# Performance work log

Measured on AMD Instinct MI355X. Metric: run time of the kernel, lower is better.

The kernel has to match this reference:

```python
import jax, jax.numpy as jnp
import numpy as np

B = 1_000_000
D = 6
IU = jnp.triu_indices(D)  # upper-triangular index pair for 21-vector packing


def _make_pd_trivec(key, batch):
    # random PD covariance -> packed upper-triangular 21-vector
    A = 0.3 * jax.random.normal(key, (batch, D, D), dtype=jnp.float32)
    S = jnp.einsum('bij,bkj->bik', A, A) + jnp.eye(D, dtype=jnp.float32)
    return S[:, IU[0], IU[1]]  # [B, 21]


def _vec_to_sym(v):
    # [B,21] -> symmetric [B,6,6]
    M = jnp.zeros((v.shape[0], D, D), dtype=v.dtype).at[:, IU[0], IU[1]].set(v)
    diag = jnp.einsum('bii->bi', M)
    return M + jnp.swapaxes(M, -1, -2) - jnp.einsum('bi,ij->bij', diag, jnp.eye(D, dtype=v.dtype))


def setup_inputs() -> dict:
    key = jax.random.key(0)
    kt, kp = jax.random.split(key)
    return {
        'target': _make_pd_trivec(kt, B),
        'pred': _make_pd_trivec(kp, B),
    }


def reference(target, pred):
    # Huber loss (delta=1, mean reduction) on the packed vectors
    d = pred - target
    ad = jnp.abs(d)
    l1 = jnp.mean(jnp.where(ad < 1.0, 0.5 * d * d, ad - 0.5))

    eps_eye = 1e-5 * jnp.eye(D, dtype=pred.dtype)
    P = _vec_to_sym(pred) + eps_eye    # [B,6,6]
    T = _vec_to_sym(target) + eps_eye  # [B,6,6]

    # KL(N(0,P) || N(0,T)) = 0.5*(tr(T^-1 P) - 6 + logdet T - logdet P)
    Lp = jnp.linalg.cholesky(P)
    Lt = jnp.linalg.cholesky(T)
    solve = jax.vmap(lambda a, b: jax.scipy.linalg.solve_triangular(a, b, lower=True))
    M = solve(Lt, Lp)                               # Lt^{-1} Lp, [B,6,6]
    tr = jnp.sum(M * M, axis=(-1, -2))              # tr(T^-1 P)
    logdet_t = 2.0 * jnp.sum(jnp.log(jnp.einsum('bii->bi', Lt)), axis=-1)
    logdet_p = 2.0 * jnp.sum(jnp.log(jnp.einsum('bii->bi', Lp)), axis=-1)
    kl = 0.5 * (tr - D + logdet_t - logdet_p)

    return jnp.mean(kl) + l1
```

## Files before the change

kernel.cpp:

```cpp
#include <hip/hip_runtime.h>
#include <hip/hip_bf16.h>

#define B_TOTAL 1000000
#define NBLK2 ((B_TOTAL + 511) / 512)

typedef float f4u __attribute__((ext_vector_type(4), aligned(4)));

__device__ __forceinline__ constexpr int up_idx(int i, int j) {
    return i * 6 - i * (i - 1) / 2 + (j - i);
}

__device__ __forceinline__ void load21(const float* __restrict__ src, float* dst) {
#pragma unroll
    for (int q = 0; q < 5; ++q) {
        f4u v = *reinterpret_cast<const f4u*>(src + 4 * q);
        dst[4 * q + 0] = v[0]; dst[4 * q + 1] = v[1];
        dst[4 * q + 2] = v[2]; dst[4 * q + 3] = v[3];
    }
    dst[20] = src[20];
}

__device__ __forceinline__ void chol6(const float* v, float L[6][6], float dinv[6]) {
#pragma unroll
    for (int j = 0; j < 6; ++j) {
        float s = v[up_idx(j, j)] + 1e-5f;
#pragma unroll
        for (int k = 0; k < 6; ++k)
            if (k < j) s -= L[j][k] * L[j][k];
        float r = __builtin_amdgcn_rsqf(s);
        L[j][j] = s * r;
        dinv[j] = r;
#pragma unroll
        for (int i = 0; i < 6; ++i)
            if (i > j) {
                float a = v[up_idx(j, i)];
#pragma unroll
                for (int k = 0; k < 6; ++k)
                    if (k < j) a -= L[i][k] * L[j][k];
                L[i][j] = a * r;
            }
    }
}

__device__ __forceinline__ float element_loss(const float* t, const float* p) {
    float hs = 0.0f;
#pragma unroll
    for (int k = 0; k < 21; ++k) {
        float d = p[k] - t[k];
        float ad = fabsf(d);
        hs += (ad < 1.0f) ? 0.5f * d * d : ad - 0.5f;
    }

    float Lt[6][6], Lp[6][6], dti[6], dpi[6];
    chol6(t, Lt, dti);
    chol6(p, Lp, dpi);

    float tr = 0.0f;
#pragma unroll
    for (int c = 0; c < 6; ++c) {
        float m[6];
#pragma unroll
        for (int r = 0; r < 6; ++r)
            if (r >= c) {
                float s = Lp[r][c];
#pragma unroll
                for (int k = 0; k < 6; ++k)
                    if (k >= c && k < r) s -= Lt[r][k] * m[k];
                m[r] = s * dti[r];
                tr += m[r] * m[r];
            }
    }

    float ratio = 1.0f;
#pragma unroll
    for (int i = 0; i < 6; ++i) ratio *= Lt[i][i] * dpi[i];
    float kl = 0.5f * (tr - 6.0f) + 0.69314718056f * __builtin_amdgcn_logf(ratio);

    return kl + hs * (1.0f / 21.0f);
}

__global__ void __launch_bounds__(256) kl_huber_kernel(const float* __restrict__ target,
                                                       const float* __restrict__ pred,
                                                       double* __restrict__ partial) {
    const int tid = threadIdx.x;
    const long base = (long)blockIdx.x * 512;
    const long b0 = base + tid;
    const long b1 = base + 256 + tid;
    const bool valid0 = b0 < B_TOTAL;
    const bool valid1 = b1 < B_TOTAL;

    float t0[21], p0[21], t1[21], p1[21];
    if (valid0) {
        load21(target + b0 * 21, t0);
        load21(pred + b0 * 21, p0);
    }
    if (valid1) {
        load21(target + b1 * 21, t1);
        load21(pred + b1 * 21, p1);
    }

    float contrib = 0.0f;
    if (valid0) contrib += element_loss(t0, p0);
    if (valid1) contrib += element_loss(t1, p1);

#pragma unroll
    for (int off = 32; off > 0; off >>= 1) contrib += __shfl_down(contrib, off);

    __shared__ float wsum[4];
    int lane = tid & 63;
    int wid = tid >> 6;
    if (lane == 0) wsum[wid] = contrib;
    __syncthreads();
    if (tid == 0) {
        partial[blockIdx.x] = (double)(wsum[0] + wsum[1] + wsum[2] + wsum[3]);
    }
}

__global__ void __launch_bounds__(256) reduce_kernel(const double* __restrict__ partial,
                                                     float* __restrict__ out) {
    double s = 0.0;
    for (int i = threadIdx.x; i < NBLK2; i += 256) s += partial[i];
#pragma unroll
    for (int off = 32; off > 0; off >>= 1) s += __shfl_down(s, off);

    __shared__ double wsum[4];
    int lane = threadIdx.x & 63;
    int wid = threadIdx.x >> 6;
    if (lane == 0) wsum[wid] = s;
    __syncthreads();
    if (threadIdx.x == 0) {
        double total = wsum[0] + wsum[1] + wsum[2] + wsum[3];
        out[0] = (float)(total / (double)B_TOTAL);
    }
}

extern "C" void kernel_launch(void* const* d_in, const int* in_sizes, int n_in,
                              void* d_out, int out_size, void* d_ws, size_t ws_size,
                              hipStream_t stream) {
    const float* target = (const float*)d_in[0];
    const float* pred = (const float*)d_in[1];
    double* partial = (double*)d_ws;

    kl_huber_kernel<<<NBLK2, 256, 0, stream>>>(target, pred, partial);
    reduce_kernel<<<1, 256, 0, stream>>>(partial, (float*)d_out);
}
```

Measured before the change: 34.63 us.

## Process one element per thread with single-wavefront blocks

Each thread now handles one batch element instead of two, and blocks shrink to a single 64-lane wavefront, so the shared-memory cross-wave reduction and barrier go away. This lowers per-thread register demand and is meant to raise occupancy and latency hiding on loads. In exchange there are eight times more partial sums, so the single-block final reduction does more serial work.

```diff
diff --git a/kernel.cpp b/kernel.cpp
--- a/kernel.cpp
+++ b/kernel.cpp
@@ -2,7 +2,7 @@
 #include <hip/hip_bf16.h>
 
 #define B_TOTAL 1000000
-#define NBLK2 ((B_TOTAL + 511) / 512)
+#define NBLK64 ((B_TOTAL + 63) / 64)
 
 typedef float f4u __attribute__((ext_vector_type(4), aligned(4)));
 
@@ -79,47 +79,29 @@
     return kl + hs * (1.0f / 21.0f);
 }
 
-__global__ void __launch_bounds__(256) kl_huber_kernel(const float* __restrict__ target,
-                                                       const float* __restrict__ pred,
-                                                       double* __restrict__ partial) {
+__global__ void __launch_bounds__(64) kl_huber_kernel(const float* __restrict__ target,
+                                                      const float* __restrict__ pred,
+                                                      double* __restrict__ partial) {
     const int tid = threadIdx.x;
-    const long base = (long)blockIdx.x * 512;
-    const long b0 = base + tid;
-    const long b1 = base + 256 + tid;
-    const bool valid0 = b0 < B_TOTAL;
-    const bool valid1 = b1 < B_TOTAL;
-
-    float t0[21], p0[21], t1[21], p1[21];
-    if (valid0) {
-        load21(target + b0 * 21, t0);
-        load21(pred + b0 * 21, p0);
+    const long b = (long)blockIdx.x * 64 + tid;
+    float contrib = 0.0f;
+    if (b < B_TOTAL) {
+        float t[21], p[21];
+        load21(target + b * 21, t);
+        load21(pred + b * 21, p);
+        contrib = element_loss(t, p);
     }
-    if (valid1) {
-        load21(target + b1 * 21, t1);
-        load21(pred + b1 * 21, p1);
-    }
-
-    float contrib = 0.0f;
-    if (valid0) contrib += element_loss(t0, p0);
-    if (valid1) contrib += element_loss(t1, p1);
 
 #pragma unroll
     for (int off = 32; off > 0; off >>= 1) contrib += __shfl_down(contrib, off);
 
-    __shared__ float wsum[4];
-    int lane = tid & 63;
-    int wid = tid >> 6;
-    if (lane == 0) wsum[wid] = contrib;
-    __syncthreads();
-    if (tid == 0) {
-        partial[blockIdx.x] = (double)(wsum[0] + wsum[1] + wsum[2] + wsum[3]);
-    }
+    if (tid == 0) partial[blockIdx.x] = (double)contrib;
 }
 
 __global__ void __launch_bounds__(256) reduce_kernel(const double* __restrict__ partial,
                                                      float* __restrict__ out) {
     double s = 0.0;
-    for (int i = threadIdx.x; i < NBLK2; i += 256) s += partial[i];
+    for (int i = threadIdx.x; i < NBLK64; i += 256) s += partial[i];
 #pragma unroll
     for (int off = 32; off > 0; off >>= 1) s += __shfl_down(s, off);
 
@@ -141,6 +123,6 @@
     const float* pred = (const float*)d_in[1];
     double* partial = (double*)d_ws;
 
-    kl_huber_kernel<<<NBLK2, 256, 0, stream>>>(target, pred, partial);
+    kl_huber_kernel<<<NBLK64, 64, 0, stream>>>(target, pred, partial);
     reduce_kernel<<<1, 256, 0, stream>>>(partial, (float*)d_out);
 }
```

New measurement: 47.45 us. +37.0%, slower.
